# Optimization experiments

Measured on AMD Instinct MI355X. Metric: run time of the kernel, lower is better.

## Reference

```python
import jax, jax.numpy as jnp
import numpy as np

GRID_SIZE = 3
SPLINE_ORDER = 3
GRID_RANGE = (-1.0, 1.0)


def make_grid():
    # extended knot vector, shape (1, grid_size + 2*spline_order + 1) = (1, 10)
    h = (GRID_RANGE[1] - GRID_RANGE[0]) / GRID_SIZE
    pts = np.arange(-SPLINE_ORDER, GRID_SIZE + SPLINE_ORDER + 1, dtype=np.float32) * h + GRID_RANGE[0]
    return jnp.asarray(pts[None, :])  # broadcasts over in_features


def b_splines(x, grid):
    # x: (B, in) -> bases: (B, in, grid_size + spline_order)
    x = x[..., None]  # (B, in, 1)
    bases = ((x >= grid[:, :-1]) & (x < grid[:, 1:])).astype(x.dtype)
    for k in range(1, SPLINE_ORDER + 1):
        left = (x - grid[:, : -(k + 1)]) / (grid[:, k:-1] - grid[:, : -(k + 1)])
        right = (grid[:, k + 1:] - x) / (grid[:, k + 1:] - grid[:, 1:-k])
        bases = left * bases[..., :-1] + right * bases[..., 1:]
    return bases


def kan_linear(x, base_w, spline_w, scaler, grid):
    # efficient-kan KANLinear: silu(x)@base_w.T + b_splines(x) contracted with scaled spline weights
    base_out = jnp.einsum('bi,oi->bo', jax.nn.silu(x), base_w)
    bases = b_splines(x, grid)  # (B, in, 6)
    spline_out = jnp.einsum('bik,oik->bo', bases, spline_w * scaler[..., None])
    return base_out + spline_out


def layer_norm(x, gamma, beta, eps=1e-5):
    mu = jnp.mean(x, axis=-1, keepdims=True)
    var = jnp.mean(jnp.square(x - mu), axis=-1, keepdims=True)
    return (x - mu) * jax.lax.rsqrt(var + eps) * gamma + beta


def setup_inputs() -> dict:
    key = jax.random.key(0)
    ks = jax.random.split(key, 8)
    B, D_IN, D_HID, D_OUT = 16384, 1280, 512, 229
    NB = GRID_SIZE + SPLINE_ORDER  # 6 basis functions per input feature
    s1 = 1.0 / np.sqrt(D_IN)
    s2 = 1.0 / np.sqrt(D_HID)
    return {
        'x': jax.random.normal(ks[0], (B, D_IN), dtype=jnp.float32),
        'base_w1': jax.random.normal(ks[1], (D_HID, D_IN), dtype=jnp.float32) * s1,
        'spline_w1': jax.random.normal(ks[2], (D_HID, D_IN, NB), dtype=jnp.float32) * s1,
        'scaler1': jax.random.normal(ks[3], (D_HID, D_IN), dtype=jnp.float32) * 0.1 + 1.0,
        'ln_gamma': jnp.ones((D_HID,), dtype=jnp.float32),
        'ln_beta': jnp.zeros((D_HID,), dtype=jnp.float32),
        'base_w2': jax.random.normal(ks[4], (D_OUT, D_HID), dtype=jnp.float32) * s2,
        'spline_w2': jax.random.normal(ks[5], (D_OUT, D_HID, NB), dtype=jnp.float32) * s2,
        'scaler2': jax.random.normal(ks[6], (D_OUT, D_HID), dtype=jnp.float32) * 0.1 + 1.0,
    }


def reference(x, base_w1, spline_w1, scaler1, ln_gamma, ln_beta, base_w2, spline_w2, scaler2):
    grid = make_grid()
    h = kan_linear(x, base_w1, spline_w1, scaler1, grid)   # (B, 512)
    h = layer_norm(h, ln_gamma, ln_beta)                    # dropout: identity at inference
    out = kan_linear(h, base_w2, spline_w2, scaler2, grid)  # (B, 229)
    return out
```

## Files before the change

kernel.cpp:

```cpp
#include <hip/hip_runtime.h>


typedef short s16x8 __attribute__((ext_vector_type(8)));
typedef float f32x4 __attribute__((ext_vector_type(4)));

__device__ __forceinline__ void dma16(const void* g, void* l) {
  __builtin_amdgcn_global_load_lds(
      (const __attribute__((address_space(1))) unsigned int*)g,
      (__attribute__((address_space(3))) unsigned int*)l, 16, 0, 0);
}

__device__ __forceinline__ unsigned pk2(float lo, float hi) {
  unsigned a = __float_as_uint(lo), b = __float_as_uint(hi);
  a = a + 0x7fffu + ((a >> 16) & 1u);
  b = b + 0x7fffu + ((b >> 16) & 1u);
  return __builtin_amdgcn_perm(b, a, 0x07060302u);
}

__device__ __forceinline__ unsigned short f2bf(float f) {
  unsigned u = __float_as_uint(f);
  unsigned r = u + 0x7fffu + ((u >> 16) & 1u);
  return (unsigned short)(r >> 16);
}

__device__ __forceinline__ uint4 kan_act8(float x) {
  float e = __expf(-x);
  float s = x * __builtin_amdgcn_rcpf(1.0f + e);
  float u = fmaf(x, 1.5f, 4.5f);
  float d[10];
#pragma unroll
  for (int j = 0; j < 10; ++j) d[j] = u - (float)j;
  float b1[8];
#pragma unroll
  for (int j = 0; j < 8; ++j) b1[j] = fmaxf(0.0f, 1.0f - fabsf(d[j + 1]));
  float B2[7];
#pragma unroll
  for (int j = 0; j < 7; ++j) B2[j] = d[j] * b1[j] - d[j + 3] * b1[j + 1];
  float b3[6];
#pragma unroll
  for (int j = 0; j < 6; ++j)
    b3[j] = (d[j] * B2[j] - d[j + 4] * B2[j + 1]) * (1.0f / 6.0f);
  uint4 r;
  r.x = pk2(s, b3[0]);
  r.y = pk2(b3[1], b3[2]);
  r.z = pk2(b3[3], b3[4]);
  r.w = pk2(b3[5], 0.0f);
  return r;
}

__global__ __launch_bounds__(256) void prep_w(
    const float* __restrict__ base_w, const float* __restrict__ spline_w,
    const float* __restrict__ scaler, short* __restrict__ Wp,
    int F, int Nvalid) {
  int i = blockIdx.x * 256 + threadIdx.x;
  int n = blockIdx.y;
  if (i >= F) return;
  s16x8 v;
#pragma unroll
  for (int k = 0; k < 8; ++k) v[k] = 0;
  if (n < Nvalid) {
    int idx = n * F + i;
    float sc = scaler[idx];
    v[0] = (short)f2bf(base_w[idx]);
#pragma unroll
    for (int k = 0; k < 6; ++k) v[1 + k] = (short)f2bf(spline_w[idx * 6 + k] * sc);
  }
  int p = (i & ~3) | ((i & 3) ^ (n & 3));
  *(s16x8*)&Wp[((size_t)n * F + p) * 8] = v;
}

template <int BN>
__global__ __launch_bounds__(256, 2) void kan_gemm(
    const float* __restrict__ X, const short* __restrict__ W,
    float* __restrict__ Cp, int F, int span, long long pstride,
    int ldc, int ncols) {
  constexpr int NT = BN / 64;
  constexpr int IE = BN / 64;
  __shared__ __align__(16) short As[2][64 * 32];
  __shared__ __align__(16) short Bs[2][BN * 32];

  const int t    = threadIdx.x;
  const int lane = t & 63;
  const int w    = t >> 6;
  const int m0   = blockIdx.x * 64;
  const int f0   = blockIdx.z * span;

  const int wcol = w * (BN / 4);
  const int mrow = lane & 15;
  const int q    = lane >> 4;
  const int qs   = (q ^ (mrow & 3)) * 8;

  int a_off[4], b_off[NT];
#pragma unroll
  for (int it = 0; it < 4; ++it)
    a_off[it] = (it * 16 + mrow) * 32 + qs;
#pragma unroll
  for (int jt = 0; jt < NT; ++jt)
    b_off[jt] = (wcol + jt * 16 + mrow) * 32 + qs;

  const int sr = t >> 2, sj = t & 3;
  const float* xq = X + (size_t)(m0 + sr) * F + f0 + sj;
  const int aw = sr * 32 + ((sj ^ (sr & 3)) * 8);

  const int drow = w * (BN / 4) + (lane >> 2);
  const int dchk = lane & 3;
  const char* wg = (const char*)W + ((size_t)drow * F + f0 + dchk) * 16;
  const size_t gistr = (size_t)16 * F * 16;

  f32x4 acc[4][NT] = {};
  const int nsteps = span >> 2;

  float xn = *xq;
#pragma unroll
  for (int e = 0; e < IE; ++e)
    dma16(wg + e * gistr, &Bs[0][(w * (BN / 4) + e * 16) * 32]);
  {
    uint4 av = kan_act8(xn);
    *(uint4*)&As[0][aw] = av;
  }
  if (nsteps > 1) xn = xq[4];
  __syncthreads();

  for (int ks = 0; ks < nsteps; ++ks) {
    const int cb = ks & 1, nb = cb ^ 1;
    const bool more = (ks + 1 < nsteps);
    if (more) {
#pragma unroll
      for (int e = 0; e < IE; ++e)
        dma16(wg + (size_t)(ks + 1) * 64 + e * gistr,
              &Bs[nb][(w * (BN / 4) + e * 16) * 32]);
    }

    s16x8 af[4], bfr[NT];
#pragma unroll
    for (int it = 0; it < 4; ++it)
      af[it] = *(const s16x8*)&As[cb][a_off[it]];
#pragma unroll
    for (int jt = 0; jt < NT; ++jt)
      bfr[jt] = *(const s16x8*)&Bs[cb][b_off[jt]];
#pragma unroll
    for (int b = 0; b < NT; ++b)
#pragma unroll
      for (int a = 0; a < 4; ++a)
        acc[a][b] = __builtin_amdgcn_mfma_f32_16x16x32_bf16(
            af[a], bfr[b], acc[a][b], 0, 0, 0);

    if (more) {
      uint4 av = kan_act8(xn);
      *(uint4*)&As[nb][aw] = av;
      if (ks + 2 < nsteps) xn = xq[(size_t)(ks + 2) * 4];
    }
    __syncthreads();
  }

  float* cpt = Cp + (size_t)blockIdx.z * (size_t)pstride;
#pragma unroll
  for (int a = 0; a < 4; ++a) {
#pragma unroll
    for (int b = 0; b < NT; ++b) {
      int col = wcol + b * 16 + mrow;
      if (col < ncols) {
#pragma unroll
        for (int r = 0; r < 4; ++r) {
          int row = m0 + a * 16 + q * 4 + r;
          cpt[(size_t)row * ldc + col] = acc[a][b][r];
        }
      }
    }
  }
}

__global__ __launch_bounds__(256) void ln_reduce(
    const float* __restrict__ p0, const float* __restrict__ p1,
    float* __restrict__ h, const float* __restrict__ gamma,
    const float* __restrict__ beta, int nparts) {
  int lane = threadIdx.x & 63;
  int wv   = threadIdx.x >> 6;
  int row  = blockIdx.x * 4 + wv;
  size_t base = (size_t)row * 512 + lane * 8;
  f32x4 v0 = *(const f32x4*)(p0 + base);
  f32x4 v1 = *(const f32x4*)(p0 + base + 4);
  if (nparts == 2) {
    f32x4 u0 = *(const f32x4*)(p1 + base);
    f32x4 u1 = *(const f32x4*)(p1 + base + 4);
#pragma unroll
    for (int k = 0; k < 4; ++k) { v0[k] += u0[k]; v1[k] += u1[k]; }
  }
  float s = 0.f, s2 = 0.f;
#pragma unroll
  for (int k = 0; k < 4; ++k) { s += v0[k] + v1[k]; s2 += v0[k]*v0[k] + v1[k]*v1[k]; }
#pragma unroll
  for (int m = 32; m >= 1; m >>= 1) {
    s  += __shfl_xor(s,  m, 64);
    s2 += __shfl_xor(s2, m, 64);
  }
  float mean = s * (1.0f / 512.0f);
  float var  = s2 * (1.0f / 512.0f) - mean * mean;
  float rstd = rsqrtf(var + 1e-5f);
  const f32x4 g0 = *(const f32x4*)(gamma + lane * 8);
  const f32x4 g1 = *(const f32x4*)(gamma + lane * 8 + 4);
  const f32x4 be0 = *(const f32x4*)(beta + lane * 8);
  const f32x4 be1 = *(const f32x4*)(beta + lane * 8 + 4);
#pragma unroll
  for (int k = 0; k < 4; ++k) {
    v0[k] = (v0[k] - mean) * rstd * g0[k] + be0[k];
    v1[k] = (v1[k] - mean) * rstd * g1[k] + be1[k];
  }
  *(f32x4*)(h + base) = v0;
  *(f32x4*)(h + base + 4) = v1;
}

__global__ __launch_bounds__(256) void out_reduce(
    const float* __restrict__ p0, const float* __restrict__ p1,
    float* __restrict__ out, int nparts) {
  int idx = blockIdx.x * 256 + threadIdx.x;
  int row = idx >> 8;
  int c   = idx & 255;
  float v = p0[idx];
  if (nparts == 2) v += p1[idx];
  if (c < 229) out[(size_t)row * 229 + c] = v;
}

extern "C" void kernel_launch(void* const* d_in, const int* in_sizes, int n_in,
                              void* d_out, int out_size, void* d_ws, size_t ws_size,
                              hipStream_t stream) {
  const float* x         = (const float*)d_in[0];
  const float* base_w1   = (const float*)d_in[1];
  const float* spline_w1 = (const float*)d_in[2];
  const float* scaler1   = (const float*)d_in[3];
  const float* ln_gamma  = (const float*)d_in[4];
  const float* ln_beta   = (const float*)d_in[5];
  const float* base_w2   = (const float*)d_in[6];
  const float* spline_w2 = (const float*)d_in[7];
  const float* scaler2   = (const float*)d_in[8];
  float* out = (float*)d_out;

  const int B = 16384, D_IN = 1280, D_HID = 512, D_OUT = 229;

  const size_t szW1 = (size_t)D_HID * D_IN * 8 * 2;
  const size_t szW2 = (size_t)256 * D_HID * 8 * 2;
  const size_t szH  = (size_t)B * D_HID * 4;
  const size_t szP  = (size_t)B * 512 * 4;
  char* ws = (char*)d_ws;
  short* W1p = (short*)ws;
  short* W2p = (short*)(ws + szW1);
  float* h   = (float*)(ws + szW1 + szW2);
  float* p0  = (float*)(ws + szW1 + szW2 + szH);
  float* p1  = (float*)(ws + szW1 + szW2 + szH + szP);

  const int parts = (ws_size >= szW1 + szW2 + szH + 2 * szP) ? 2 : 1;
  const long long pstride = (long long)(szP / 4);

  prep_w<<<dim3(D_IN / 256, D_HID), 256, 0, stream>>>(
      base_w1, spline_w1, scaler1, W1p, D_IN, D_HID);
  prep_w<<<dim3(D_HID / 256, 256), 256, 0, stream>>>(
      base_w2, spline_w2, scaler2, W2p, D_HID, D_OUT);

  kan_gemm<512><<<dim3(B / 64, 1, parts), 256, 0, stream>>>(
      x, W1p, p0, D_IN, D_IN / parts, pstride, D_HID, D_HID);

  ln_reduce<<<dim3(B / 4), 256, 0, stream>>>(p0, p1, h, ln_gamma, ln_beta, parts);

  kan_gemm<256><<<dim3(B / 64, 1, parts), 256, 0, stream>>>(
      h, W2p, p0, D_HID, D_HID / parts, pstride, 256, 256);

  out_reduce<<<dim3(B * 256 / 256), 256, 0, stream>>>(p0, p1, out, parts);
}
```

Before: 442.3 us.

## Replace LDS-staged GEMM with register-direct 32x32 MFMA tiles

Rewrites the KAN GEMM so it no longer stages tiles through LDS. Each wave now computes spline activations in registers and loads transposed bf16 weights straight from global memory into 32x32x16 MFMA operands. Blocks grow to 512 threads covering 128 rows, with loose periodic barriers kept so waves stay roughly in step for cache reuse. The 1/6 basis factor moves into the weight prep step. This removes LDS traffic and per-step syncs, but each wave now fetches the full weight set from L2 with no cross-wave sharing, which raises global load pressure.

```diff
diff --git a/kernel.cpp b/kernel.cpp
--- a/kernel.cpp
+++ b/kernel.cpp
@@ -3,12 +3,7 @@
 
 typedef short s16x8 __attribute__((ext_vector_type(8)));
 typedef float f32x4 __attribute__((ext_vector_type(4)));
-
-__device__ __forceinline__ void dma16(const void* g, void* l) {
-  __builtin_amdgcn_global_load_lds(
-      (const __attribute__((address_space(1))) unsigned int*)g,
-      (__attribute__((address_space(3))) unsigned int*)l, 16, 0, 0);
-}
+typedef float f32x16 __attribute__((ext_vector_type(16)));
 
 __device__ __forceinline__ unsigned pk2(float lo, float hi) {
   unsigned a = __float_as_uint(lo), b = __float_as_uint(hi);
@@ -23,7 +18,7 @@
   return (unsigned short)(r >> 16);
 }
 
-__device__ __forceinline__ uint4 kan_act8(float x) {
+__device__ __forceinline__ s16x8 kan_act8(float x) {
   float e = __expf(-x);
   float s = x * __builtin_amdgcn_rcpf(1.0f + e);
   float u = fmaf(x, 1.5f, 4.5f);
@@ -39,19 +34,19 @@
   float b3[6];
 #pragma unroll
   for (int j = 0; j < 6; ++j)
-    b3[j] = (d[j] * B2[j] - d[j + 4] * B2[j + 1]) * (1.0f / 6.0f);
-  uint4 r;
-  r.x = pk2(s, b3[0]);
-  r.y = pk2(b3[1], b3[2]);
-  r.z = pk2(b3[3], b3[4]);
-  r.w = pk2(b3[5], 0.0f);
-  return r;
+    b3[j] = d[j] * B2[j] - d[j + 4] * B2[j + 1];
+  union { uint4 u4; s16x8 v; } r;
+  r.u4.x = pk2(s, b3[0]);
+  r.u4.y = pk2(b3[1], b3[2]);
+  r.u4.z = pk2(b3[3], b3[4]);
+  r.u4.w = pk2(b3[5], 0.0f);
+  return r.v;
 }
 
 __global__ __launch_bounds__(256) void prep_w(
     const float* __restrict__ base_w, const float* __restrict__ spline_w,
-    const float* __restrict__ scaler, short* __restrict__ Wp,
-    int F, int Nvalid) {
+    const float* __restrict__ scaler, short* __restrict__ WT,
+    int F, int Ncols, int Nvalid) {
   int i = blockIdx.x * 256 + threadIdx.x;
   int n = blockIdx.y;
   if (i >= F) return;
@@ -60,112 +55,70 @@
   for (int k = 0; k < 8; ++k) v[k] = 0;
   if (n < Nvalid) {
     int idx = n * F + i;
-    float sc = scaler[idx];
+    float sc = scaler[idx] * (1.0f / 6.0f);
     v[0] = (short)f2bf(base_w[idx]);
 #pragma unroll
     for (int k = 0; k < 6; ++k) v[1 + k] = (short)f2bf(spline_w[idx * 6 + k] * sc);
   }
-  int p = (i & ~3) | ((i & 3) ^ (n & 3));
-  *(s16x8*)&Wp[((size_t)n * F + p) * 8] = v;
-}
-
-template <int BN>
-__global__ __launch_bounds__(256, 2) void kan_gemm(
-    const float* __restrict__ X, const short* __restrict__ W,
-    float* __restrict__ Cp, int F, int span, long long pstride,
-    int ldc, int ncols) {
-  constexpr int NT = BN / 64;
-  constexpr int IE = BN / 64;
-  __shared__ __align__(16) short As[2][64 * 32];
-  __shared__ __align__(16) short Bs[2][BN * 32];
-
+  *(s16x8*)&WT[((size_t)i * Ncols + n) * 8] = v;
+}
+
+template <int NT>
+__global__ __launch_bounds__(512, 2) void kan_gemm(
+    const float* __restrict__ X, const short* __restrict__ WT,
+    float* __restrict__ Cp, int F, int span, long long pstride, int ldc) {
+  constexpr int Ncols = NT * 64;
   const int t    = threadIdx.x;
   const int lane = t & 63;
   const int w    = t >> 6;
-  const int m0   = blockIdx.x * 64;
+  const int wm   = w >> 1;
+  const int wn   = w & 1;
+  const int r5   = lane & 31;
+  const int hi   = lane >> 5;
+  const int m0   = blockIdx.x * 128 + wm * 32;
+  const int c0   = wn * (NT * 32);
   const int f0   = blockIdx.z * span;
 
-  const int wcol = w * (BN / 4);
-  const int mrow = lane & 15;
-  const int q    = lane >> 4;
-  const int qs   = (q ^ (mrow & 3)) * 8;
-
-  int a_off[4], b_off[NT];
-#pragma unroll
-  for (int it = 0; it < 4; ++it)
-    a_off[it] = (it * 16 + mrow) * 32 + qs;
-#pragma unroll
-  for (int jt = 0; jt < NT; ++jt)
-    b_off[jt] = (wcol + jt * 16 + mrow) * 32 + qs;
-
-  const int sr = t >> 2, sj = t & 3;
-  const float* xq = X + (size_t)(m0 + sr) * F + f0 + sj;
-  const int aw = sr * 32 + ((sj ^ (sr & 3)) * 8);
-
-  const int drow = w * (BN / 4) + (lane >> 2);
-  const int dchk = lane & 3;
-  const char* wg = (const char*)W + ((size_t)drow * F + f0 + dchk) * 16;
-  const size_t gistr = (size_t)16 * F * 16;
-
-  f32x4 acc[4][NT] = {};
+  const s16x8* wpt = (const s16x8*)WT + (size_t)(f0 + hi) * Ncols + c0 + r5;
+  const f32x4* xq = (const f32x4*)(X + (size_t)(m0 + r5) * F + f0);
+
+  f32x16 acc[NT] = {};
   const int nsteps = span >> 2;
 
-  float xn = *xq;
-#pragma unroll
-  for (int e = 0; e < IE; ++e)
-    dma16(wg + e * gistr, &Bs[0][(w * (BN / 4) + e * 16) * 32]);
-  {
-    uint4 av = kan_act8(xn);
-    *(uint4*)&As[0][aw] = av;
-  }
-  if (nsteps > 1) xn = xq[4];
-  __syncthreads();
-
+  f32x4 xv = xq[0];
   for (int ks = 0; ks < nsteps; ++ks) {
-    const int cb = ks & 1, nb = cb ^ 1;
-    const bool more = (ks + 1 < nsteps);
-    if (more) {
-#pragma unroll
-      for (int e = 0; e < IE; ++e)
-        dma16(wg + (size_t)(ks + 1) * 64 + e * gistr,
-              &Bs[nb][(w * (BN / 4) + e * 16) * 32]);
-    }
-
-    s16x8 af[4], bfr[NT];
-#pragma unroll
-    for (int it = 0; it < 4; ++it)
-      af[it] = *(const s16x8*)&As[cb][a_off[it]];
-#pragma unroll
-    for (int jt = 0; jt < NT; ++jt)
-      bfr[jt] = *(const s16x8*)&Bs[cb][b_off[jt]];
-#pragma unroll
-    for (int b = 0; b < NT; ++b)
-#pragma unroll
-      for (int a = 0; a < 4; ++a)
-        acc[a][b] = __builtin_amdgcn_mfma_f32_16x16x32_bf16(
-            af[a], bfr[b], acc[a][b], 0, 0, 0);
-
-    if (more) {
-      uint4 av = kan_act8(xn);
-      *(uint4*)&As[nb][aw] = av;
-      if (ks + 2 < nsteps) xn = xq[(size_t)(ks + 2) * 4];
-    }
-    __syncthreads();
+    f32x4 xn;
+    if (ks + 1 < nsteps) xn = xq[ks + 1];
+
+    s16x8 b0[NT];
+#pragma unroll
+    for (int nt = 0; nt < NT; ++nt) b0[nt] = wpt[nt * 32];
+    s16x8 a0 = kan_act8(xv[hi]);
+#pragma unroll
+    for (int nt = 0; nt < NT; ++nt)
+      acc[nt] = __builtin_amdgcn_mfma_f32_32x32x16_bf16(a0, b0[nt], acc[nt], 0, 0, 0);
+
+    s16x8 b1[NT];
+#pragma unroll
+    for (int nt = 0; nt < NT; ++nt) b1[nt] = wpt[2 * Ncols + nt * 32];
+    s16x8 a1 = kan_act8(xv[2 + hi]);
+#pragma unroll
+    for (int nt = 0; nt < NT; ++nt)
+      acc[nt] = __builtin_amdgcn_mfma_f32_32x32x16_bf16(a1, b1[nt], acc[nt], 0, 0, 0);
+
+    wpt += (size_t)4 * Ncols;
+    xv = xn;
+    if ((ks & 7) == 7) __builtin_amdgcn_s_barrier();
   }
 
   float* cpt = Cp + (size_t)blockIdx.z * (size_t)pstride;
 #pragma unroll
-  for (int a = 0; a < 4; ++a) {
-#pragma unroll
-    for (int b = 0; b < NT; ++b) {
-      int col = wcol + b * 16 + mrow;
-      if (col < ncols) {
-#pragma unroll
-        for (int r = 0; r < 4; ++r) {
-          int row = m0 + a * 16 + q * 4 + r;
-          cpt[(size_t)row * ldc + col] = acc[a][b][r];
-        }
-      }
+  for (int nt = 0; nt < NT; ++nt) {
+    int col = c0 + nt * 32 + r5;
+#pragma unroll
+    for (int reg = 0; reg < 16; ++reg) {
+      int row = m0 + (reg & 3) + 8 * (reg >> 2) + 4 * hi;
+      cpt[(size_t)row * ldc + col] = acc[nt][reg];
     }
   }
 }
@@ -237,8 +190,8 @@
 
   const int B = 16384, D_IN = 1280, D_HID = 512, D_OUT = 229;
 
-  const size_t szW1 = (size_t)D_HID * D_IN * 8 * 2;
-  const size_t szW2 = (size_t)256 * D_HID * 8 * 2;
+  const size_t szW1 = (size_t)D_IN * D_HID * 8 * 2;
+  const size_t szW2 = (size_t)D_HID * 256 * 8 * 2;
   const size_t szH  = (size_t)B * D_HID * 4;
   const size_t szP  = (size_t)B * 512 * 4;
   char* ws = (char*)d_ws;
@@ -252,17 +205,17 @@
   const long long pstride = (long long)(szP / 4);
 
   prep_w<<<dim3(D_IN / 256, D_HID), 256, 0, stream>>>(
-      base_w1, spline_w1, scaler1, W1p, D_IN, D_HID);
+      base_w1, spline_w1, scaler1, W1p, D_IN, D_HID, D_HID);
   prep_w<<<dim3(D_HID / 256, 256), 256, 0, stream>>>(
-      base_w2, spline_w2, scaler2, W2p, D_HID, D_OUT);
-
-  kan_gemm<512><<<dim3(B / 64, 1, parts), 256, 0, stream>>>(
-      x, W1p, p0, D_IN, D_IN / parts, pstride, D_HID, D_HID);
+      base_w2, spline_w2, scaler2, W2p, D_HID, 256, D_OUT);
+
+  kan_gemm<8><<<dim3(B / 128, 1, parts), 512, 0, stream>>>(
+      x, W1p, p0, D_IN, D_IN / parts, pstride, D_HID);
 
   ln_reduce<<<dim3(B / 4), 256, 0, stream>>>(p0, p1, h, ln_gamma, ln_beta, parts);
 
-  kan_gemm<256><<<dim3(B / 64, 1, parts), 256, 0, stream>>>(
-      h, W2p, p0, D_HID, D_HID / parts, pstride, 256, 256);
+  kan_gemm<4><<<dim3(B / 128, 1, parts), 512, 0, stream>>>(
+      h, W2p, p0, D_HID, D_HID / parts, pstride, 256);
 
   out_reduce<<<dim3(B * 256 / 256), 256, 0, stream>>>(p0, p1, out, parts);
 }
```

Result: slower. 664.7 us (+50.3%).
